# Kernel tuning notes

Measured on AMD Instinct MI355X. Metric: run time of the kernel, lower is better.

Reference implementation:

```python
import jax, jax.numpy as jnp
import numpy as np

B, L, H = 2, 2048, 2048
DI, N, DTR, K = 4096, 16, 128, 4  # intermediate, state, dt_rank, conv kernel


def setup_inputs() -> dict:
    key = jax.random.key(0)
    ks = jax.random.split(key, 8)
    x = jax.random.normal(ks[0], (B, L, H), jnp.float32)
    in_proj_w = jax.random.normal(ks[1], (2 * DI, H), jnp.float32) * 0.02
    conv1d_w = jax.random.normal(ks[2], (DI, 1, K), jnp.float32) * 0.1
    conv1d_b = jnp.zeros((DI,), jnp.float32)
    x_proj_w = jax.random.normal(ks[3], (DTR + 2 * N, DI), jnp.float32) * 0.02
    bound = DTR ** -0.5
    dt_proj_w = jax.random.uniform(ks[4], (DI, DTR), jnp.float32, -bound, bound)
    # faithful dt bias init: inverse-softplus of dt ~ Uniform-log[0.001, 0.1]
    dt = jnp.exp(jax.random.uniform(ks[5], (DI,), jnp.float32)
                 * (np.log(0.1) - np.log(0.001)) + np.log(0.001))
    dt = jnp.clip(dt, 1e-4)
    dt_proj_b = dt + jnp.log(-jnp.expm1(-dt))
    A_log = jnp.log(jnp.broadcast_to(jnp.arange(1, N + 1, dtype=jnp.float32), (DI, N)))
    D = jnp.ones((DI,), jnp.float32)
    out_proj_w = jax.random.normal(ks[6], (H, DI), jnp.float32) * 0.02
    return dict(x=x, in_proj_w=in_proj_w, conv1d_w=conv1d_w, conv1d_b=conv1d_b,
                x_proj_w=x_proj_w, dt_proj_w=dt_proj_w, dt_proj_b=dt_proj_b,
                A_log=A_log, D=D, out_proj_w=out_proj_w)


def _mamba_forward(x, in_proj_w, conv1d_w, conv1d_b, x_proj_w,
                   dt_proj_w, dt_proj_b, A_log, D, out_proj_w):
    # in_proj -> split into ssm input and gate (res)
    x_and_res = jnp.einsum('blh,eh->ble', x, in_proj_w)          # [B,L,2*DI]
    xi, res = jnp.split(x_and_res, 2, axis=-1)                    # [B,L,DI] each

    # depthwise causal conv1d (kernel K, left-pad K-1, truncated to L)
    xc = jnp.transpose(xi, (0, 2, 1))                             # [B,DI,L]
    xc = jax.lax.conv_general_dilated(
        xc, conv1d_w, window_strides=(1,), padding=((K - 1, 0),),
        dimension_numbers=('NCH', 'OIH', 'NCH'), feature_group_count=DI)
    xc = xc + conv1d_b[None, :, None]
    u = jax.nn.silu(jnp.transpose(xc, (0, 2, 1)))                 # [B,L,DI]

    # selective SSM parameters
    A = -jnp.exp(A_log.astype(jnp.float32))                       # [DI,N]
    x_dbl = jnp.einsum('bld,ed->ble', u, x_proj_w)                # [B,L,DTR+2N]
    dlt, Bm, Cm = jnp.split(x_dbl, [DTR, DTR + N], axis=-1)
    delta = jax.nn.softplus(jnp.einsum('blr,dr->bld', dlt, dt_proj_w) + dt_proj_b)

    # selective scan over time; carry h: [B,DI,N]
    def step(h, inp):
        d_t, B_t, C_t, u_t = inp                                  # [B,DI],[B,N],[B,N],[B,DI]
        dA = jnp.exp(d_t[:, :, None] * A)                         # [B,DI,N]
        h = dA * h + d_t[:, :, None] * B_t[:, None, :] * u_t[:, :, None]
        y_t = jnp.einsum('bdn,bn->bd', h, C_t)
        return h, y_t

    xs = (jnp.transpose(delta, (1, 0, 2)), jnp.transpose(Bm, (1, 0, 2)),
          jnp.transpose(Cm, (1, 0, 2)), jnp.transpose(u, (1, 0, 2)))
    h0 = jnp.zeros((x.shape[0], DI, N), jnp.float32)
    _, ys = jax.lax.scan(step, h0, xs)                            # ys: [L,B,DI]
    y = jnp.transpose(ys, (1, 0, 2)) + u * D.astype(jnp.float32)  # skip via D

    y = y * jax.nn.silu(res)                                      # gate
    return jnp.einsum('bld,hd->blh', y, out_proj_w)               # [B,L,H]


def reference(x, in_proj_w, conv1d_w, conv1d_b, x_proj_w,
              dt_proj_w, dt_proj_b, A_log, D, out_proj_w):
    return _mamba_forward(x, in_proj_w, conv1d_w, conv1d_b, x_proj_w,
                          dt_proj_w, dt_proj_b, A_log, D, out_proj_w)
```

## Files before the change

### kernel.cpp

```cpp
#include <hip/hip_runtime.h>
#include <hip/hip_bf16.h>
#include <stdint.h>

#define DEV static __device__ __forceinline__

typedef __attribute__((ext_vector_type(8))) short short8;
typedef __attribute__((ext_vector_type(4))) float f32x4;
typedef __attribute__((address_space(3))) void lds_void;
typedef __attribute__((address_space(1))) void glb_void;

constexpr int CB = 2, CL = 2048, CH = 2048, CDI = 4096, CN = 16, CDTR = 128;
constexpr int BLR = CB * CL;
constexpr int NC = 32, LC = 64;
constexpr int KSL = 8;

DEV ushort f2b(float f) {
  union { float f; uint32_t u; } v; v.f = f;
  uint32_t u = v.u;
  return (ushort)((u + 0x7fffu + ((u >> 16) & 1u)) >> 16);
}
DEV float b2f(ushort b) {
  union { uint32_t u; float f; } v; v.u = ((uint32_t)b) << 16;
  return v.f;
}
DEV void gload16(const ushort* g, ushort* l) {
  __builtin_amdgcn_global_load_lds((const glb_void*)g, (lds_void*)l, 16, 0, 0);
}
DEV f32x4 mfma16(short8 a, short8 b, f32x4 c) {
  return __builtin_amdgcn_mfma_f32_16x16x32_bf16(a, b, c, 0, 0, 0);
}

__global__ void cast_kernel(const float* __restrict__ in, ushort* __restrict__ out, int n4) {
  int i = blockIdx.x * blockDim.x + threadIdx.x;
  if (i >= n4) return;
  float4 v = *(const float4*)(in + (size_t)i * 4);
  *(ushort4*)(out + (size_t)i * 4) = make_ushort4(f2b(v.x), f2b(v.y), f2b(v.z), f2b(v.w));
}

__global__ void cast_pad_xproj_kernel(const float* __restrict__ in, ushort* __restrict__ out) {
  int i = blockIdx.x * blockDim.x + threadIdx.x;
  if (i >= (256 * 4096 / 4)) return;
  int idx = i * 4;
  int r = idx >> 12;
  ushort4 o;
  if (r < 160) {
    float4 v = *(const float4*)(in + idx);
    o = make_ushort4(f2b(v.x), f2b(v.y), f2b(v.z), f2b(v.w));
  } else {
    o = make_ushort4(0, 0, 0, 0);
  }
  *(ushort4*)(out + idx) = o;
}

__global__ void conv_silu_kernel(const ushort* __restrict__ xr, const float* __restrict__ w,
                                 const float* __restrict__ bias, ushort* __restrict__ u) {
  int t = blockIdx.x * blockDim.x + threadIdx.x;
  if (t >= BLR * CDI / 2) return;
  int d2 = t & (CDI / 2 - 1);
  int bl = t >> 11;
  int l = bl & (CL - 1);
  int d = d2 << 1;
  float4 w0 = *(const float4*)(w + (size_t)d * 4);
  float4 w1 = *(const float4*)(w + (size_t)d * 4 + 4);
  float wa0[4] = {w0.x, w0.y, w0.z, w0.w};
  float wa1[4] = {w1.x, w1.y, w1.z, w1.w};
  float a0 = bias[d], a1 = bias[d + 1];
#pragma unroll
  for (int k = 0; k < 4; ++k) {
    int ls = l - 3 + k;
    if (ls >= 0) {
      ushort2 xv = *(const ushort2*)(xr + (size_t)(bl - 3 + k) * 8192 + d);
      a0 = fmaf(wa0[k], b2f(xv.x), a0);
      a1 = fmaf(wa1[k], b2f(xv.y), a1);
    }
  }
  float s0 = a0 / (1.f + __expf(-a0));
  float s1 = a1 / (1.f + __expf(-a1));
  *(ushort2*)(u + (size_t)bl * 4096 + d) = make_ushort2(f2b(s0), f2b(s1));
}

template<int EPI>
__global__ __launch_bounds__(256, 4)
void gemm_bt_kernel(const ushort* __restrict__ A, const ushort* __restrict__ Bw,
                    void* __restrict__ Cp, const float* __restrict__ bias,
                    int M, int N, int K) {
  __shared__ ushort sA[128 * 32];
  __shared__ ushort sB[128 * 32];
  const int tid = threadIdx.x;
  const int bm = blockIdx.x, bn = blockIdx.y;
  const int w = tid >> 6, l = tid & 63;
  const int wr = w >> 1, wc = w & 1;
  const int q = l >> 4, r = l & 15;

  f32x4 acc[4][4] = {};

  const ushort* Ab = A + (size_t)bm * 128 * K;
  const ushort* Bb = Bw + (size_t)bn * 128 * K;
  const int nk = K >> 5;
  for (int kt = 0; kt < nk; ++kt) {
    const int k0 = kt << 5;
#pragma unroll
    for (int i = 0; i < 2; ++i) {
      const int chunk = i * 256 + tid;
      const int row = chunk >> 2;
      const int cofs = (chunk & 3) << 3;
      gload16(Ab + (size_t)row * K + k0 + cofs, sA + chunk * 8);
      gload16(Bb + (size_t)row * K + k0 + cofs, sB + chunk * 8);
    }
    __syncthreads();
    short8 af[4], bfg[4];
#pragma unroll
    for (int i = 0; i < 4; ++i) {
      af[i]  = *(const short8*)(sA + (wr * 64 + i * 16 + r) * 32 + q * 8);
      bfg[i] = *(const short8*)(sB + (wc * 64 + i * 16 + r) * 32 + q * 8);
    }
#pragma unroll
    for (int i = 0; i < 4; ++i)
#pragma unroll
      for (int j = 0; j < 4; ++j)
        acc[i][j] = mfma16(af[i], bfg[j], acc[i][j]);
    __syncthreads();
  }

  const int m0 = bm * 128 + wr * 64;
  const int n0 = bn * 128 + wc * 64;
#pragma unroll
  for (int i = 0; i < 4; ++i) {
#pragma unroll
    for (int j = 0; j < 4; ++j) {
#pragma unroll
      for (int v = 0; v < 4; ++v) {
        const int grow = m0 + i * 16 + q * 4 + v;
        const int gcol = n0 + j * 16 + r;
        const float val = acc[i][j][v];
        if (EPI == 0) {
          ((ushort*)Cp)[(size_t)grow * N + gcol] = f2b(val);
        } else if (EPI == 1) {
          ((float*)Cp)[(size_t)grow * N + gcol] = val;
        } else {
          float xv = val + bias[gcol];
          float sp = xv > 20.f ? xv : log1pf(__expf(xv));
          ((ushort*)Cp)[(size_t)grow * N + gcol] = f2b(sp);
        }
      }
    }
  }
}

template<int EPI>
__global__ __launch_bounds__(512, 1)
void gemm256p_kernel(const ushort* __restrict__ A, const ushort* __restrict__ Bw,
                     void* __restrict__ Cp, int N, int K) {
  __shared__ ushort sA[2][16384];
  __shared__ ushort sB[2][16384];
  const int tid = threadIdx.x;
  const int bm = blockIdx.x, bn = blockIdx.y;
  const int wid = tid >> 6, l = tid & 63;
  const int wr = wid >> 2, wc = wid & 3;
  const int q = l >> 4, r = l & 15;
  const int rx = r & 7;
  const int nt = K >> 6;

  const ushort* Ab = A + (size_t)bm * 256 * K;
  const ushort* Bb = Bw + (size_t)bn * 256 * K;

  const int srow = tid >> 3;
  const int sxor = (tid & 7) ^ (srow & 7);

  auto stageA = [&](int T, int j) {
    const int Ts = (T < nt) ? T : (nt - 1);
    gload16(Ab + (size_t)(j * 64 + srow) * K + Ts * 64 + sxor * 8,
            &sA[T & 1][0] + j * 4096 + tid * 8);
  };
  auto stageB = [&](int T, int j) {
    const int Ts = (T < nt) ? T : (nt - 1);
    gload16(Bb + (size_t)(j * 64 + srow) * K + Ts * 64 + sxor * 8,
            &sB[T & 1][0] + j * 4096 + tid * 8);
  };

  const int sl0 = (q ^ rx) * 8;
  const int sl1 = ((4 + q) ^ rx) * 8;

  f32x4 acc[8][4] = {};

  stageA(0, 1); stageA(0, 3);
  stageB(0, 0); stageA(0, 0);
  stageB(0, 2); stageA(0, 2);
  stageB(0, 1); stageB(0, 3);
  stageA(1, 1); stageA(1, 3);
  asm volatile("s_waitcnt vmcnt(2)" ::: "memory");
  __builtin_amdgcn_s_barrier();

#define PHASE(M0, M1, S0, S1, LAST)                                        \
  {                                                                        \
    const int ra0 = (wr * 128 + (M0) * 16 + r) * 64;                       \
    const int ra1 = (wr * 128 + (M1) * 16 + r) * 64;                       \
    short8 a00 = *(const short8*)(At + ra0 + sl0);                         \
    short8 a01 = *(const short8*)(At + ra0 + sl1);                         \
    short8 a10 = *(const short8*)(At + ra1 + sl0);                         \
    short8 a11 = *(const short8*)(At + ra1 + sl1);                         \
    S0; S1;                                                                \
    if (LAST) asm volatile("s_waitcnt vmcnt(2)" ::: "memory");             \
    __builtin_amdgcn_s_barrier();                                          \
    asm volatile("s_waitcnt lgkmcnt(0)" ::: "memory");                     \
    __builtin_amdgcn_sched_barrier(0);                                     \
    __builtin_amdgcn_s_setprio(1);                                         \
    _Pragma("unroll")                                                      \
    for (int n = 0; n < 4; ++n) {                                          \
      acc[M0][n] = mfma16(a00, bf[n][0], acc[M0][n]);                      \
      acc[M0][n] = mfma16(a01, bf[n][1], acc[M0][n]);                      \
      acc[M1][n] = mfma16(a10, bf[n][0], acc[M1][n]);                      \
      acc[M1][n] = mfma16(a11, bf[n][1], acc[M1][n]);                      \
    }                                                                      \
    __builtin_amdgcn_s_setprio(0);                                         \
    __builtin_amdgcn_sched_barrier(0);                                     \
    __builtin_amdgcn_s_barrier();                                          \
  }

  for (int t = 0; t < nt; ++t) {
    const ushort* At = &sA[t & 1][0];
    const ushort* Bt = &sB[t & 1][0];
    short8 bf[4][2];
#pragma unroll
    for (int n = 0; n < 4; ++n) {
      const int br = (wc * 64 + n * 16 + r) * 64;
      bf[n][0] = *(const short8*)(Bt + br + sl0);
      bf[n][1] = *(const short8*)(Bt + br + sl1);
    }
    PHASE(6, 7, stageB(t + 1, 0), stageA(t + 1, 0), false)
    PHASE(4, 5, stageB(t + 1, 2), stageA(t + 1, 2), false)
    PHASE(2, 3, stageB(t + 1, 1), stageB(t + 1, 3), false)
    PHASE(0, 1, stageA(t + 2, 1), stageA(t + 2, 3), true)
  }
#undef PHASE

  const int m0g = bm * 256 + wr * 128;
  const int n0g = bn * 256 + wc * 64;
#pragma unroll
  for (int m = 0; m < 8; ++m)
#pragma unroll
    for (int n = 0; n < 4; ++n)
#pragma unroll
      for (int v = 0; v < 4; ++v) {
        const int grow = m0g + m * 16 + q * 4 + v;
        const int gcol = n0g + n * 16 + r;
        if (EPI == 0) ((ushort*)Cp)[(size_t)grow * N + gcol] = f2b(acc[m][n][v]);
        else          ((float*)Cp)[(size_t)grow * N + gcol]  = acc[m][n][v];
      }
}

__global__ __launch_bounds__(256, 4)
void gemm_btk_kernel(const ushort* __restrict__ A, const ushort* __restrict__ Bw,
                     float* __restrict__ Cpart, int N, int Ktot, int Ksl) {
  __shared__ ushort sA[128 * 32];
  __shared__ ushort sB[128 * 32];
  const int tid = threadIdx.x;
  const int bm = blockIdx.x, bn = blockIdx.y, z = blockIdx.z;
  const int w = tid >> 6, l = tid & 63;
  const int wr = w >> 1, wc = w & 1;
  const int q = l >> 4, r = l & 15;

  f32x4 acc[4][4] = {};

  const ushort* Ab = A + (size_t)bm * 128 * Ktot + z * Ksl;
  const ushort* Bb = Bw + (size_t)bn * 128 * Ktot + z * Ksl;
  const int nk = Ksl >> 5;
  for (int kt = 0; kt < nk; ++kt) {
    const int k0 = kt << 5;
#pragma unroll
    for (int i = 0; i < 2; ++i) {
      const int chunk = i * 256 + tid;
      const int row = chunk >> 2;
      const int cofs = (chunk & 3) << 3;
      gload16(Ab + (size_t)row * Ktot + k0 + cofs, sA + chunk * 8);
      gload16(Bb + (size_t)row * Ktot + k0 + cofs, sB + chunk * 8);
    }
    __syncthreads();
    short8 af[4], bfg[4];
#pragma unroll
    for (int i = 0; i < 4; ++i) {
      af[i]  = *(const short8*)(sA + (wr * 64 + i * 16 + r) * 32 + q * 8);
      bfg[i] = *(const short8*)(sB + (wc * 64 + i * 16 + r) * 32 + q * 8);
    }
#pragma unroll
    for (int i = 0; i < 4; ++i)
#pragma unroll
      for (int j = 0; j < 4; ++j)
        acc[i][j] = mfma16(af[i], bfg[j], acc[i][j]);
    __syncthreads();
  }

  float* Cz = Cpart + (size_t)z * BLR * N;
  const int m0 = bm * 128 + wr * 64;
  const int n0 = bn * 128 + wc * 64;
#pragma unroll
  for (int i = 0; i < 4; ++i)
#pragma unroll
    for (int j = 0; j < 4; ++j)
#pragma unroll
      for (int v = 0; v < 4; ++v)
        Cz[(size_t)(m0 + i * 16 + q * 4 + v) * N + (n0 + j * 16 + r)] = acc[i][j][v];
}

__global__ __launch_bounds__(256)
void reduce_xdbl_kernel(const float* __restrict__ part, float* __restrict__ xdbl,
                        ushort* __restrict__ dlt) {
  const int i = blockIdx.x * 256 + threadIdx.x;
  const int idx = i * 4;
  const int row = idx >> 8, col = idx & 255;
  float4 s = make_float4(0.f, 0.f, 0.f, 0.f);
#pragma unroll
  for (int z = 0; z < KSL; ++z) {
    float4 v = *(const float4*)(part + (size_t)z * BLR * 256 + idx);
    s.x += v.x; s.y += v.y; s.z += v.z; s.w += v.w;
  }
  *(float4*)(xdbl + idx) = s;
  if (col < 128) {
    *(ushort4*)(dlt + (size_t)row * 128 + col) =
        make_ushort4(f2b(s.x), f2b(s.y), f2b(s.z), f2b(s.w));
  }
}

__global__ __launch_bounds__(256)
void scan_pass1_kernel(const ushort* __restrict__ delta_bf, const ushort* __restrict__ u_bf,
                       const float* __restrict__ xdbl, const float* __restrict__ A_log,
                       float* __restrict__ Hc, float* __restrict__ Ssum) {
  __shared__ float4 sB[LC * 4];
  const int blk = blockIdx.x;
  const int dblk = blk & 15, bc = blk >> 4;
  const int b = bc & (CB - 1), c = bc >> 1;
  const int tid = threadIdx.x;
  const int d = dblk * 256 + tid;
  const size_t rowbase = (size_t)b * CL + c * LC;

  {
    const int rr = tid >> 2, seg = tid & 3;
    sB[tid] = *(const float4*)(xdbl + (rowbase + rr) * 256 + 128 + seg * 4);
  }
  __syncthreads();

  float Ae[16];
#pragma unroll
  for (int n = 0; n < 16; ++n) Ae[n] = -__expf(A_log[(size_t)d * CN + n]);
  float h[16] = {};
  float S = 0.f;
  for (int t = 0; t < LC; ++t) {
    const float dl = b2f(delta_bf[(rowbase + t) * 4096 + d]);
    const float uu = b2f(u_bf[(rowbase + t) * 4096 + d]);
    const float du = dl * uu;
    S += dl;
#pragma unroll
    for (int q = 0; q < 4; ++q) {
      float4 bq = sB[t * 4 + q];
      h[q * 4 + 0] = __expf(Ae[q * 4 + 0] * dl) * h[q * 4 + 0] + du * bq.x;
      h[q * 4 + 1] = __expf(Ae[q * 4 + 1] * dl) * h[q * 4 + 1] + du * bq.y;
      h[q * 4 + 2] = __expf(Ae[q * 4 + 2] * dl) * h[q * 4 + 2] + du * bq.z;
      h[q * 4 + 3] = __expf(Ae[q * 4 + 3] * dl) * h[q * 4 + 3] + du * bq.w;
    }
  }
  float4* Hp = (float4*)(Hc + ((((size_t)c * CB + b) * CDI + d) << 4));
#pragma unroll
  for (int q = 0; q < 4; ++q)
    Hp[q] = make_float4(h[q * 4 + 0], h[q * 4 + 1], h[q * 4 + 2], h[q * 4 + 3]);
  Ssum[((size_t)c * CB + b) * CDI + d] = S;
}

__global__ __launch_bounds__(256)
void scan_pass2_kernel(float* __restrict__ Hc, const float* __restrict__ Ssum,
                       const float* __restrict__ A_log) {
  const int t = blockIdx.x * 256 + threadIdx.x;
  const int n = t & 15, d = (t >> 4) & (CDI - 1), b = t >> 16;
  const float Ae = -__expf(A_log[(size_t)d * CN + n]);
  float h = 0.f;
  for (int c = 1; c < NC; ++c) {
    const size_t idxp = ((size_t)(c - 1) * CB + b) * CDI + d;
    const float P = __expf(Ae * Ssum[idxp]);
    h = P * h + Hc[idxp * 16 + n];
    Hc[idxp * 16 + n] = h;
  }
}

__global__ __launch_bounds__(256)
void scan_pass3_kernel(const ushort* __restrict__ delta_bf, const ushort* __restrict__ u_bf,
                       const float* __restrict__ xdbl, const ushort* __restrict__ xr,
                       const float* __restrict__ A_log, const float* __restrict__ Dvec,
                       const float* __restrict__ Hc, ushort* __restrict__ ybf) {
  __shared__ float4 sB[LC * 4];
  __shared__ float4 sC[LC * 4];
  const int blk = blockIdx.x;
  const int dblk = blk & 15, bc = blk >> 4;
  const int b = bc & (CB - 1), c = bc >> 1;
  const int tid = threadIdx.x;
  const int d = dblk * 256 + tid;
  const size_t rowbase = (size_t)b * CL + c * LC;

  {
    const int rr = tid >> 2, seg = tid & 3;
    sB[tid] = *(const float4*)(xdbl + (rowbase + rr) * 256 + 128 + seg * 4);
    sC[tid] = *(const float4*)(xdbl + (rowbase + rr) * 256 + 144 + seg * 4);
  }
  __syncthreads();

  float Ae[16];
#pragma unroll
  for (int n = 0; n < 16; ++n) Ae[n] = -__expf(A_log[(size_t)d * CN + n]);
  float h[16];
  if (c == 0) {
#pragma unroll
    for (int n = 0; n < 16; ++n) h[n] = 0.f;
  } else {
    const float4* Hp = (const float4*)(Hc + ((((size_t)(c - 1) * CB + b) * CDI + d) << 4));
#pragma unroll
    for (int q = 0; q < 4; ++q) {
      float4 hv = Hp[q];
      h[q * 4 + 0] = hv.x; h[q * 4 + 1] = hv.y; h[q * 4 + 2] = hv.z; h[q * 4 + 3] = hv.w;
    }
  }
  const float Dd = Dvec[d];
  for (int t = 0; t < LC; ++t) {
    const float dl = b2f(delta_bf[(rowbase + t) * 4096 + d]);
    const float uu = b2f(u_bf[(rowbase + t) * 4096 + d]);
    const float du = dl * uu;
    float y = 0.f;
#pragma unroll
    for (int q = 0; q < 4; ++q) {
      float4 bq = sB[t * 4 + q];
      float4 cq = sC[t * 4 + q];
      h[q * 4 + 0] = __expf(Ae[q * 4 + 0] * dl) * h[q * 4 + 0] + du * bq.x;
      h[q * 4 + 1] = __expf(Ae[q * 4 + 1] * dl) * h[q * 4 + 1] + du * bq.y;
      h[q * 4 + 2] = __expf(Ae[q * 4 + 2] * dl) * h[q * 4 + 2] + du * bq.z;
      h[q * 4 + 3] = __expf(Ae[q * 4 + 3] * dl) * h[q * 4 + 3] + du * bq.w;
      y = fmaf(h[q * 4 + 0], cq.x, y);
      y = fmaf(h[q * 4 + 1], cq.y, y);
      y = fmaf(h[q * 4 + 2], cq.z, y);
      y = fmaf(h[q * 4 + 3], cq.w, y);
    }
    const float res = b2f(xr[(rowbase + t) * 8192 + 4096 + d]);
    const float sres = res / (1.f + __expf(-res));
    ybf[(rowbase + t) * 4096 + d] = f2b((y + uu * Dd) * sres);
  }
}

extern "C" void kernel_launch(void* const* d_in, const int* in_sizes, int n_in,
                              void* d_out, int out_size, void* d_ws, size_t ws_size,
                              hipStream_t stream) {
  (void)in_sizes; (void)n_in; (void)out_size; (void)ws_size;
  const float* x       = (const float*)d_in[0];
  const float* in_w    = (const float*)d_in[1];
  const float* conv_w  = (const float*)d_in[2];
  const float* conv_b  = (const float*)d_in[3];
  const float* xproj_w = (const float*)d_in[4];
  const float* dt_w    = (const float*)d_in[5];
  const float* dt_b    = (const float*)d_in[6];
  const float* A_log   = (const float*)d_in[7];
  const float* Dvec    = (const float*)d_in[8];
  const float* out_w   = (const float*)d_in[9];
  float* out = (float*)d_out;
  char* ws = (char*)d_ws;
  const size_t MB = 1u << 20;

  ushort* xb    = (ushort*)(ws);
  float*  Hc    = (float*)(ws);
  ushort* wout  = (ushort*)(ws);
  ushort* wb1   = (ushort*)(ws + 16 * MB);
  ushort* u_bf  = (ushort*)(ws + 16 * MB);
  ushort* xr    = (ushort*)(ws + 48 * MB);
  float*  part  = (float*)(ws + 112 * MB);
  ushort* delta = (ushort*)(ws + 112 * MB);
  ushort* ybf   = (ushort*)(ws + 144 * MB);
  float*  xdbl  = (float*)(ws + 176 * MB);
  ushort* dlt   = (ushort*)(ws + 180 * MB);
  ushort* wxp   = (ushort*)(ws + 181 * MB);
  ushort* wdt   = (ushort*)(ws + 183 * MB);
  float*  Ssum  = (float*)(ws + 184 * MB);

  auto cast = [&](const float* in, ushort* o, int n) {
    cast_kernel<<<(n / 4 + 255) / 256, 256, 0, stream>>>(in, o, n / 4);
  };

  cast(x, xb, BLR * CH);
  cast(in_w, wb1, 2 * CDI * CH);
  gemm256p_kernel<0><<<dim3(BLR / 256, (2 * CDI) / 256), 512, 0, stream>>>(
      xb, wb1, xr, 2 * CDI, CH);
  conv_silu_kernel<<<(BLR * CDI / 2) / 256, 256, 0, stream>>>(xr, conv_w, conv_b, u_bf);
  cast_pad_xproj_kernel<<<(256 * 4096 / 4) / 256, 256, 0, stream>>>(xproj_w, wxp);
  gemm_btk_kernel<<<dim3(BLR / 128, 2, KSL), 256, 0, stream>>>(
      u_bf, wxp, part, 256, CDI, CDI / KSL);
  reduce_xdbl_kernel<<<(BLR * 256 / 4) / 256, 256, 0, stream>>>(part, xdbl, dlt);
  cast(dt_w, wdt, CDI * CDTR);
  gemm_bt_kernel<2><<<dim3(BLR / 128, CDI / 128), 256, 0, stream>>>(
      dlt, wdt, delta, dt_b, BLR, CDI, CDTR);
  scan_pass1_kernel<<<NC * CB * (CDI / 256), 256, 0, stream>>>(
      delta, u_bf, xdbl, A_log, Hc, Ssum);
  scan_pass2_kernel<<<(CB * CDI * CN) / 256, 256, 0, stream>>>(Hc, Ssum, A_log);
  scan_pass3_kernel<<<NC * CB * (CDI / 256), 256, 0, stream>>>(
      delta, u_bf, xdbl, xr, A_log, Dvec, Hc, ybf);
  cast(out_w, wout, CH * CDI);
  gemm_bt_kernel<1><<<dim3(BLR / 128, CH / 128), 256, 0, stream>>>(
      ybf, wout, out, nullptr, BLR, CH, CDI);
}
```

Before: 547.2 us.

## Use 256x128 double-buffered GEMM for out_proj and vectorize conv_silu

Replaces the out_proj GEMM (128x128 tiles, 256 threads) with a new 512-thread kernel using 256x128 tiles, a K-step of 64, swizzled LDS double-buffering via direct global-to-LDS loads, and phased MFMA issue with priority hints. This cuts redundant operand loads and overlaps loads with compute. Separately, the conv+SiLU kernel now handles 8 channels per thread with 16-byte loads and stores instead of 2. The new GEMM launches only 16x16 blocks at one block per CU, which may leave the machine underfilled.

```diff
diff --git a/kernel.cpp b/kernel.cpp
--- a/kernel.cpp
+++ b/kernel.cpp
@@ -55,28 +55,39 @@
 __global__ void conv_silu_kernel(const ushort* __restrict__ xr, const float* __restrict__ w,
                                  const float* __restrict__ bias, ushort* __restrict__ u) {
   int t = blockIdx.x * blockDim.x + threadIdx.x;
-  if (t >= BLR * CDI / 2) return;
-  int d2 = t & (CDI / 2 - 1);
-  int bl = t >> 11;
-  int l = bl & (CL - 1);
-  int d = d2 << 1;
-  float4 w0 = *(const float4*)(w + (size_t)d * 4);
-  float4 w1 = *(const float4*)(w + (size_t)d * 4 + 4);
-  float wa0[4] = {w0.x, w0.y, w0.z, w0.w};
-  float wa1[4] = {w1.x, w1.y, w1.z, w1.w};
-  float a0 = bias[d], a1 = bias[d + 1];
+  if (t >= BLR * CDI / 8) return;
+  const int d8 = (t & (CDI / 8 - 1)) << 3;
+  const int bl = t >> 9;
+  const int l = bl & (CL - 1);
+  float a[8];
+  {
+    float4 b0 = *(const float4*)(bias + d8);
+    float4 b1 = *(const float4*)(bias + d8 + 4);
+    a[0] = b0.x; a[1] = b0.y; a[2] = b0.z; a[3] = b0.w;
+    a[4] = b1.x; a[5] = b1.y; a[6] = b1.z; a[7] = b1.w;
+  }
+  float wk[8][4];
+#pragma unroll
+  for (int j = 0; j < 8; ++j) {
+    float4 wj = *(const float4*)(w + (size_t)(d8 + j) * 4);
+    wk[j][0] = wj.x; wk[j][1] = wj.y; wk[j][2] = wj.z; wk[j][3] = wj.w;
+  }
 #pragma unroll
   for (int k = 0; k < 4; ++k) {
-    int ls = l - 3 + k;
-    if (ls >= 0) {
-      ushort2 xv = *(const ushort2*)(xr + (size_t)(bl - 3 + k) * 8192 + d);
-      a0 = fmaf(wa0[k], b2f(xv.x), a0);
-      a1 = fmaf(wa1[k], b2f(xv.y), a1);
-    }
-  }
-  float s0 = a0 / (1.f + __expf(-a0));
-  float s1 = a1 / (1.f + __expf(-a1));
-  *(ushort2*)(u + (size_t)bl * 4096 + d) = make_ushort2(f2b(s0), f2b(s1));
+    if (l - 3 + k >= 0) {
+      short8 xv = *(const short8*)(xr + (size_t)(bl - 3 + k) * 8192 + d8);
+#pragma unroll
+      for (int j = 0; j < 8; ++j)
+        a[j] = fmaf(wk[j][k], b2f((ushort)xv[j]), a[j]);
+    }
+  }
+  short8 o;
+#pragma unroll
+  for (int j = 0; j < 8; ++j) {
+    float s = a[j] / (1.f + __expf(-a[j]));
+    o[j] = (short)f2b(s);
+  }
+  *(short8*)(u + (size_t)bl * 4096 + d8) = o;
 }
 
 template<int EPI>
@@ -249,6 +260,107 @@
       }
 }
 
+template<int EPI>
+__global__ __launch_bounds__(512, 1)
+void gemm256n_kernel(const ushort* __restrict__ A, const ushort* __restrict__ Bw,
+                     void* __restrict__ Cp, int N, int K) {
+  __shared__ ushort sA[2][16384];
+  __shared__ ushort sB[2][8192];
+  const int tid = threadIdx.x;
+  const int bm = blockIdx.x, bn = blockIdx.y;
+  const int wid = tid >> 6, l = tid & 63;
+  const int wr = wid >> 2, wc = wid & 3;
+  const int q = l >> 4, r = l & 15;
+  const int rx = r & 7;
+  const int nt = K >> 6;
+
+  const ushort* Ab = A + (size_t)bm * 256 * K;
+  const ushort* Bb = Bw + (size_t)bn * 128 * K;
+
+  const int srow = tid >> 3;
+  const int sxor = (tid & 7) ^ (srow & 7);
+
+  auto stageA = [&](int T, int j) {
+    const int Ts = (T < nt) ? T : (nt - 1);
+    gload16(Ab + (size_t)(j * 64 + srow) * K + Ts * 64 + sxor * 8,
+            &sA[T & 1][0] + j * 4096 + tid * 8);
+  };
+  auto stageB = [&](int T, int j) {
+    const int Ts = (T < nt) ? T : (nt - 1);
+    gload16(Bb + (size_t)(j * 64 + srow) * K + Ts * 64 + sxor * 8,
+            &sB[T & 1][0] + j * 4096 + tid * 8);
+  };
+
+  const int sl0 = (q ^ rx) * 8;
+  const int sl1 = ((4 + q) ^ rx) * 8;
+
+  f32x4 acc[8][2] = {};
+
+  stageA(0, 1); stageA(0, 3);
+  stageB(0, 0); stageA(0, 0);
+  stageB(0, 1); stageA(0, 2);
+  stageA(1, 1); stageA(1, 3);
+  asm volatile("s_waitcnt vmcnt(2)" ::: "memory");
+  __builtin_amdgcn_s_barrier();
+
+#define PHASE(M0, M1, S0, S1, LAST)                                        \
+  {                                                                        \
+    const int ra0 = (wr * 128 + (M0) * 16 + r) * 64;                       \
+    const int ra1 = (wr * 128 + (M1) * 16 + r) * 64;                       \
+    short8 a00 = *(const short8*)(At + ra0 + sl0);                         \
+    short8 a01 = *(const short8*)(At + ra0 + sl1);                         \
+    short8 a10 = *(const short8*)(At + ra1 + sl0);                         \
+    short8 a11 = *(const short8*)(At + ra1 + sl1);                         \
+    S0; S1;                                                                \
+    if (LAST) asm volatile("s_waitcnt vmcnt(2)" ::: "memory");             \
+    __builtin_amdgcn_s_barrier();                                          \
+    asm volatile("s_waitcnt lgkmcnt(0)" ::: "memory");                     \
+    __builtin_amdgcn_sched_barrier(0);                                     \
+    __builtin_amdgcn_s_setprio(1);                                         \
+    _Pragma("unroll")                                                      \
+    for (int n = 0; n < 2; ++n) {                                          \
+      acc[M0][n] = mfma16(a00, bf[n][0], acc[M0][n]);                      \
+      acc[M0][n] = mfma16(a01, bf[n][1], acc[M0][n]);                      \
+      acc[M1][n] = mfma16(a10, bf[n][0], acc[M1][n]);                      \
+      acc[M1][n] = mfma16(a11, bf[n][1], acc[M1][n]);                      \
+    }                                                                      \
+    __builtin_amdgcn_s_setprio(0);                                         \
+    __builtin_amdgcn_sched_barrier(0);                                     \
+    __builtin_amdgcn_s_barrier();                                          \
+  }
+
+  for (int t = 0; t < nt; ++t) {
+    const ushort* At = &sA[t & 1][0];
+    const ushort* Bt = &sB[t & 1][0];
+    short8 bf[2][2];
+#pragma unroll
+    for (int n = 0; n < 2; ++n) {
+      const int br = (wc * 32 + n * 16 + r) * 64;
+      bf[n][0] = *(const short8*)(Bt + br + sl0);
+      bf[n][1] = *(const short8*)(Bt + br + sl1);
+    }
+    PHASE(6, 7, stageB(t + 1, 0), stageA(t + 1, 0), false)
+    PHASE(4, 5, stageB(t + 1, 1), stageA(t + 1, 2), false)
+    PHASE(2, 3, , , false)
+    PHASE(0, 1, stageA(t + 2, 1), stageA(t + 2, 3), true)
+  }
+#undef PHASE
+
+  const int m0g = bm * 256 + wr * 128;
+  const int n0g = bn * 128 + wc * 32;
+#pragma unroll
+  for (int m = 0; m < 8; ++m)
+#pragma unroll
+    for (int n = 0; n < 2; ++n)
+#pragma unroll
+      for (int v = 0; v < 4; ++v) {
+        const int grow = m0g + m * 16 + q * 4 + v;
+        const int gcol = n0g + n * 16 + r;
+        if (EPI == 0) ((ushort*)Cp)[(size_t)grow * N + gcol] = f2b(acc[m][n][v]);
+        else          ((float*)Cp)[(size_t)grow * N + gcol]  = acc[m][n][v];
+      }
+}
+
 __global__ __launch_bounds__(256, 4)
 void gemm_btk_kernel(const ushort* __restrict__ A, const ushort* __restrict__ Bw,
                      float* __restrict__ Cpart, int N, int Ktot, int Ksl) {
@@ -482,7 +594,7 @@
   cast(in_w, wb1, 2 * CDI * CH);
   gemm256p_kernel<0><<<dim3(BLR / 256, (2 * CDI) / 256), 512, 0, stream>>>(
       xb, wb1, xr, 2 * CDI, CH);
-  conv_silu_kernel<<<(BLR * CDI / 2) / 256, 256, 0, stream>>>(xr, conv_w, conv_b, u_bf);
+  conv_silu_kernel<<<(BLR * CDI / 8) / 256, 256, 0, stream>>>(xr, conv_w, conv_b, u_bf);
   cast_pad_xproj_kernel<<<(256 * 4096 / 4) / 256, 256, 0, stream>>>(xproj_w, wxp);
   gemm_btk_kernel<<<dim3(BLR / 128, 2, KSL), 256, 0, stream>>>(
       u_bf, wxp, part, 256, CDI, CDI / KSL);
@@ -496,6 +608,6 @@
   scan_pass3_kernel<<<NC * CB * (CDI / 256), 256, 0, stream>>>(
       delta, u_bf, xdbl, xr, A_log, Dvec, Hc, ybf);
   cast(out_w, wout, CH * CDI);
-  gemm_bt_kernel<1><<<dim3(BLR / 128, CH / 128), 256, 0, stream>>>(
-      ybf, wout, out, nullptr, BLR, CH, CDI);
-}
+  gemm256n_kernel<1><<<dim3(BLR / 256, CH / 128), 512, 0, stream>>>(
+      ybf, wout, out, CH, CDI);
+}
```

New measurement: 558.2 us. +2.0%, slower.
